# Kernel tuning notes

Hardware: AMD Instinct MI355X
Metric: run time of the kernel (lower is better)

The kernel has to match this reference:

```python
import jax, jax.numpy as jnp
import numpy as np

B, DIM, EMBDIM = 32, 512, 512
MEMSIZE, MEMSEQ = 32, 64
VOCAB = 50257


def setup_inputs() -> dict:
    key = jax.random.key(0)
    ks = jax.random.split(key, 10)
    inp = {
        'enc': jax.random.normal(ks[0], (B, DIM), jnp.float32),
        'encsumm': jax.random.normal(ks[1], (B, DIM), jnp.float32),
        'embsumm': jax.random.normal(ks[2], (B, EMBDIM), jnp.float32),
        'memencs': jax.random.normal(ks[3], (B, MEMSIZE, MEMSEQ, DIM), jnp.float32),
        'memencsumm': jax.random.normal(ks[4], (B, MEMSIZE, MEMSEQ, DIM), jnp.float32),
        'memembsumm': jax.random.normal(ks[5], (B, MEMSIZE, MEMSEQ, EMBDIM), jnp.float32),
        'memmask': jnp.ones((B, MEMSIZE, MEMSEQ), jnp.float32),
        'memids': jax.random.randint(ks[6], (B, MEMSIZE, MEMSEQ), 0, VOCAB, jnp.int64 if jax.config.jax_enable_x64 else jnp.int32),
        'W_out': jax.random.normal(ks[7], (VOCAB, 2 * DIM), jnp.float32) * 0.02,
        'b_out': jnp.zeros((VOCAB,), jnp.float32),
        'W_mix': jax.random.normal(ks[8], (2, 2 * DIM), jnp.float32) * 0.02,
        'b_mix': jnp.zeros((2,), jnp.float32),
        'unktok_mask': jnp.ones((VOCAB,), jnp.float32),  # no unktoks
    }
    return inp


def reference(enc, encsumm, embsumm, memencs, memencsumm, memembsumm, memmask,
              memids, W_out, b_out, W_mix, b_mix, unktok_mask):
    # copy branch: attention over flattened memory, scatter-add into vocab
    query = jnp.concatenate([embsumm, jnp.zeros_like(encsumm), enc], axis=-1)        # (B, 2*dim+embdim)
    keys = jnp.concatenate([memembsumm, jnp.zeros_like(memencsumm), memencs], axis=-1)  # (B, M, Z, 2*dim+embdim)
    w = jnp.einsum('bd,bmzd->bmz', query, keys) + jnp.log(memmask)
    b = w.shape[0]
    w = w.reshape(b, -1)                                    # (B, M*Z)
    alphas = jax.nn.softmax(w, axis=-1)
    mem_flat = memencs.reshape(b, -1, memencs.shape[-1])    # (B, M*Z, dim)
    mem_enc_summ = jnp.einsum('bm,bmd->bd', alphas, mem_flat)
    toks = memids.reshape(b, -1)                            # (B, M*Z)
    rows = jnp.arange(b)[:, None]
    vocsize = W_out.shape[0]
    probs_mem = jnp.zeros((b, vocsize), alphas.dtype).at[rows, toks].add(alphas)
    # generation branch
    h = jnp.concatenate([encsumm, enc], axis=-1)            # (B, 2*dim)
    logits_gen = h @ W_out.T + b_out + jnp.log(unktok_mask)[None, :]
    probs_gen = jax.nn.softmax(logits_gen, axis=-1)
    # mixer combine
    mix = jax.nn.softmax(h @ W_mix.T + b_mix, axis=-1)      # (B, 2)
    probs = mix[:, 0:1] * probs_gen + mix[:, 1:2] * probs_mem
    # original stack/gather trick: selects probs where nonzero, zeros where zero -> identity
    probs = jnp.where(probs != 0, probs, jnp.zeros_like(probs))
    return probs, mem_enc_summ
```

## Files before the change

### kernel.cpp

```cpp
#include <hip/hip_runtime.h>
#include <hip/hip_bf16.h>

#define NB   32
#define DIMK 512
#define MM   32
#define ZZ   64
#define MZV  2048
#define VOC  50257

typedef __attribute__((ext_vector_type(8))) short  short8;
typedef __attribute__((ext_vector_type(4))) float  f32x4;
typedef __attribute__((ext_vector_type(8))) unsigned short ushort8;

#define WS_W      0
#define WS_PVEC   (WS_W + NB*MZV)
#define WS_LSTAT  (WS_PVEC + NB*MM*DIMK)
#define WS_GSTATW (WS_LSTAT + NB*MM*2)
#define WS_MIX    (WS_GSTATW + NB*2)
#define WS_GPART  (WS_MIX + NB*2)
#define WS_H      (WS_GPART + NB*32*2)

__device__ __forceinline__ ushort8 cvt8(float4 a, float4 b) {
    union { ushort8 u; __hip_bfloat162 h[4]; } r;
    r.h[0] = __float22bfloat162_rn(make_float2(a.x, a.y));
    r.h[1] = __float22bfloat162_rn(make_float2(a.z, a.w));
    r.h[2] = __float22bfloat162_rn(make_float2(b.x, b.y));
    r.h[3] = __float22bfloat162_rn(make_float2(b.z, b.w));
    return r.u;
}

typedef const __attribute__((address_space(1))) void* gas_t;
typedef __attribute__((address_space(3))) void*       las_t;
__device__ __forceinline__ void gload16(const void* g, void* l) {
    __builtin_amdgcn_global_load_lds((gas_t)g, (las_t)l, 16, 0, 0);
}

__global__ void k0_stageh(const float* __restrict__ encsumm, const float* __restrict__ enc,
                          float* __restrict__ ws)
{
    int b = blockIdx.x;
    int c = threadIdx.x * 4;
    const float* src = (c < DIMK) ? (encsumm + b*DIMK + c) : (enc + b*DIMK + (c - DIMK));
    float4 v = *(const float4*)src;
    union { ushort4 u; __hip_bfloat162 h[2]; } o;
    o.h[0] = __float22bfloat162_rn(make_float2(v.x, v.y));
    o.h[1] = __float22bfloat162_rn(make_float2(v.z, v.w));
    *(ushort4*)((unsigned short*)(ws + WS_H) + b*1024 + c) = o.u;
}

__global__ __launch_bounds__(256) void k1_mem(
    const float* __restrict__ enc, const float* __restrict__ embsumm,
    const float* __restrict__ memencs, const float* __restrict__ memembsumm,
    const float* __restrict__ memmask, float* __restrict__ ws)
{
    int blk = blockIdx.x;
    int b = blk >> 5, m = blk & 31;
    int tid = threadIdx.x, wid = tid >> 6, lane = tid & 63;
    int c0 = lane * 4, c1 = c0 + 256;
    const float* encb = enc + b * DIMK;
    const float* embb = embsumm + b * DIMK;
    float4 qe0 = *(const float4*)(encb + c0);
    float4 qe1 = *(const float4*)(encb + c1);
    float4 qm0 = *(const float4*)(embb + c0);
    float4 qm1 = *(const float4*)(embb + c1);
    const float* meb = memencs    + (long)(b*MM + m) * ZZ * DIMK;
    const float* mmb = memembsumm + (long)(b*MM + m) * ZZ * DIMK;
    const float* mkb = memmask    + (long)(b*MM + m) * ZZ;
    float* w_ws = ws + WS_W + b*MZV + m*ZZ;

    float lmax = -3.0e38f, lsum = 0.f;
    float4 a0 = make_float4(0.f,0.f,0.f,0.f), a1 = make_float4(0.f,0.f,0.f,0.f);

    for (int z = wid; z < ZZ; z += 4) {
        const float* mer = meb + z*DIMK;
        const float* mmr = mmb + z*DIMK;
        float4 e0 = *(const float4*)(mer + c0);
        float4 e1 = *(const float4*)(mer + c1);
        float4 s0 = *(const float4*)(mmr + c0);
        float4 s1 = *(const float4*)(mmr + c1);
        float d = e0.x*qe0.x + e0.y*qe0.y + e0.z*qe0.z + e0.w*qe0.w
                + e1.x*qe1.x + e1.y*qe1.y + e1.z*qe1.z + e1.w*qe1.w
                + s0.x*qm0.x + s0.y*qm0.y + s0.z*qm0.z + s0.w*qm0.w
                + s1.x*qm1.x + s1.y*qm1.y + s1.z*qm1.z + s1.w*qm1.w;
        #pragma unroll
        for (int off = 32; off; off >>= 1) d += __shfl_xor(d, off);
        d += logf(mkb[z]);
        if (lane == 0) w_ws[z] = d;
        float nm = fmaxf(lmax, d);
        float sc = __expf(lmax - nm);
        float e  = __expf(d - nm);
        lsum = lsum * sc + e;
        a0.x = a0.x*sc + e*e0.x; a0.y = a0.y*sc + e*e0.y;
        a0.z = a0.z*sc + e*e0.z; a0.w = a0.w*sc + e*e0.w;
        a1.x = a1.x*sc + e*e1.x; a1.y = a1.y*sc + e*e1.y;
        a1.z = a1.z*sc + e*e1.z; a1.w = a1.w*sc + e*e1.w;
        lmax = nm;
    }

    __shared__ float sacc[4][DIMK];
    __shared__ float sst[4][2];
    *(float4*)&sacc[wid][c0] = a0;
    *(float4*)&sacc[wid][c1] = a1;
    if (lane == 0) { sst[wid][0] = lmax; sst[wid][1] = lsum; }
    __syncthreads();
    float bm = fmaxf(fmaxf(sst[0][0], sst[1][0]), fmaxf(sst[2][0], sst[3][0]));
    float sc0 = __expf(sst[0][0]-bm), sc1 = __expf(sst[1][0]-bm);
    float sc2 = __expf(sst[2][0]-bm), sc3 = __expf(sst[3][0]-bm);
    float bs = sst[0][1]*sc0 + sst[1][1]*sc1 + sst[2][1]*sc2 + sst[3][1]*sc3;
    int d0 = tid * 2;
    float2 v0 = *(float2*)&sacc[0][d0];
    float2 v1 = *(float2*)&sacc[1][d0];
    float2 v2 = *(float2*)&sacc[2][d0];
    float2 v3 = *(float2*)&sacc[3][d0];
    float p0 = v0.x*sc0 + v1.x*sc1 + v2.x*sc2 + v3.x*sc3;
    float p1 = v0.y*sc0 + v1.y*sc1 + v2.y*sc2 + v3.y*sc3;
    float* pv = ws + WS_PVEC + (long)(b*MM+m)*DIMK + d0;
    pv[0] = p0; pv[1] = p1;
    if (tid == 0) { float* ls = ws + WS_LSTAT + (b*MM+m)*2; ls[0] = bm; ls[1] = bs; }
}

__global__ __launch_bounds__(256) void k2_comb(
    const float* __restrict__ encsumm, const float* __restrict__ enc,
    const float* __restrict__ W_mix, const float* __restrict__ b_mix,
    float* __restrict__ out, float* __restrict__ ws)
{
    int b = blockIdx.x, tid = threadIdx.x;
    const float* ls = ws + WS_LSTAT + b*MM*2;
    float gm = -3.0e38f;
    #pragma unroll
    for (int m = 0; m < MM; m++) gm = fmaxf(gm, ls[m*2]);
    float gs = 0.f;
    #pragma unroll
    for (int m = 0; m < MM; m++) gs += ls[m*2+1] * __expf(ls[m*2] - gm);
    if (tid == 0) { ws[WS_GSTATW + b*2] = gm; ws[WS_GSTATW + b*2 + 1] = gs; }
    float inv = 1.0f / gs;
    int d0 = tid * 2;
    float p0 = 0.f, p1 = 0.f;
    for (int m = 0; m < MM; m++) {
        float sc = __expf(ls[m*2] - gm);
        const float* pv = ws + WS_PVEC + (long)(b*MM+m)*DIMK + d0;
        p0 += pv[0]*sc; p1 += pv[1]*sc;
    }
    out[(long)NB*VOC + b*DIMK + d0]     = p0 * inv;
    out[(long)NB*VOC + b*DIMK + d0 + 1] = p1 * inv;

    if (tid < 64) {
        int l = tid;
        float m0 = 0.f, m1 = 0.f;
        #pragma unroll
        for (int p = 0; p < 4; p++) {
            int cc = l*4 + p*256;
            float4 h4 = (cc < 512) ? *(const float4*)(encsumm + b*DIMK + cc)
                                   : *(const float4*)(enc + b*DIMK + cc - 512);
            float4 w0 = *(const float4*)(W_mix + cc);
            float4 w1 = *(const float4*)(W_mix + 1024 + cc);
            m0 += h4.x*w0.x + h4.y*w0.y + h4.z*w0.z + h4.w*w0.w;
            m1 += h4.x*w1.x + h4.y*w1.y + h4.z*w1.z + h4.w*w1.w;
        }
        #pragma unroll
        for (int off = 32; off; off >>= 1) { m0 += __shfl_xor(m0, off); m1 += __shfl_xor(m1, off); }
        if (l == 0) {
            m0 += b_mix[0]; m1 += b_mix[1];
            float mx = fmaxf(m0, m1);
            float e0 = __expf(m0-mx), e1 = __expf(m1-mx);
            float s = e0 + e1;
            ws[WS_MIX + b*2] = e0/s; ws[WS_MIX + b*2 + 1] = e1/s;
        }
    }
}

__global__ __launch_bounds__(256, 6) void k4_gemm(
    const unsigned short* __restrict__ hbf,
    const float* __restrict__ W_out, const float* __restrict__ b_out,
    const float* __restrict__ unk, float* __restrict__ logits)
{
    __shared__ __align__(16) float          w_lds[2][32*64];
    __shared__ __align__(16) unsigned short a_lds[2][32*64];
    int tid = threadIdx.x, wid = tid >> 6, lane = tid & 63;
    int wv = wid >> 1, wb = wid & 1;
    int vt = blockIdx.x * 32;

    int idx0 = (wid*2 + 0)*64 + lane;
    int idx1 = (wid*2 + 1)*64 + lane;
    int wr0 = idx0 >> 4, wq0 = idx0 & 15;
    int wr1 = idx1 >> 4, wq1 = idx1 & 15;
    const float* wsrc0 = W_out + (long)min(vt + wr0, VOC-1)*1024 + ((wq0 ^ (wr0 & 7))*4);
    const float* wsrc1 = W_out + (long)min(vt + wr1, VOC-1)*1024 + ((wq1 ^ (wr1 & 7))*4);
    int aidx = wid*64 + lane;
    int ar = aidx >> 3, ag = aidx & 7;
    const unsigned short* asrc = hbf + ar*1024 + ((ag ^ (ar & 7))*8);

#define ISSUE(c, buf) do {                                        \
        gload16(wsrc0 + (c)*64, &w_lds[buf][idx0*4]);             \
        gload16(wsrc1 + (c)*64, &w_lds[buf][idx1*4]);             \
        gload16(asrc  + (c)*64, &a_lds[buf][aidx*8]); } while (0)

    int lg = lane >> 4, ln = lane & 15;
    int vrow = wv*16 + ln;
    int ab   = wb*16 + ln;
    f32x4 acc = {0.f, 0.f, 0.f, 0.f};

    ISSUE(0, 0);
    ISSUE(1, 1);
    __syncthreads();

    for (int c = 0; c < 16; ++c) {
        int buf = c & 1;
        #pragma unroll
        for (int s = 0; s < 2; ++s) {
            int q = s*8 + lg*2;
            float4 b0 = *(const float4*)&w_lds[buf][vrow*64 + ((q    ) ^ (vrow & 7))*4];
            float4 b1 = *(const float4*)&w_lds[buf][vrow*64 + ((q + 1) ^ (vrow & 7))*4];
            int g = s*4 + lg;
            short8 afrag = *(const short8*)&a_lds[buf][ab*64 + ((g ^ (ab & 7)))*8];
            ushort8 bu = cvt8(b0, b1);
            short8 bfrag = *(short8*)&bu;
            acc = __builtin_amdgcn_mfma_f32_16x16x32_bf16(afrag, bfrag, acc, 0, 0, 0);
        }
        __syncthreads();
        if (c + 2 < 16) ISSUE(c + 2, buf);
    }
#undef ISSUE

    int v = vt + vrow;
    if (v < VOC) {
        float bias = b_out[v] + logf(unk[v]);
        #pragma unroll
        for (int rr = 0; rr < 4; ++rr) {
            int m = wb*16 + lg*4 + rr;
            logits[(long)m*VOC + v] = acc[rr] + bias;
        }
    }
}

__global__ __launch_bounds__(256) void k5_gstat(const float* __restrict__ logits, float* __restrict__ ws)
{
    int chunk = blockIdx.x, b = blockIdx.y, tid = threadIdx.x;
    const int CH = (VOC + 31) / 32;
    int v0 = chunk * CH;
    int v1 = min(VOC, v0 + CH);
    float m = -3.0e38f, s = 0.f;
    for (int v = v0 + tid; v < v1; v += 256) {
        float x = logits[(long)b*VOC + v];
        float nm = fmaxf(m, x);
        s = s*__expf(m - nm) + __expf(x - nm);
        m = nm;
    }
    #pragma unroll
    for (int off = 32; off; off >>= 1) {
        float om = __shfl_xor(m, off), os = __shfl_xor(s, off);
        float nm = fmaxf(m, om);
        s = s*__expf(m - nm) + os*__expf(om - nm);
        m = nm;
    }
    __shared__ float sm[4], ssum[4];
    int wid = tid >> 6, lane = tid & 63;
    if (lane == 0) { sm[wid] = m; ssum[wid] = s; }
    __syncthreads();
    if (tid == 0) {
        float gm = fmaxf(fmaxf(sm[0], sm[1]), fmaxf(sm[2], sm[3]));
        float gs = ssum[0]*__expf(sm[0]-gm) + ssum[1]*__expf(sm[1]-gm)
                 + ssum[2]*__expf(sm[2]-gm) + ssum[3]*__expf(sm[3]-gm);
        ws[WS_GPART + (b*32 + chunk)*2]     = gm;
        ws[WS_GPART + (b*32 + chunk)*2 + 1] = gs;
    }
}

__global__ __launch_bounds__(256) void k6_final(float* __restrict__ probs, const float* __restrict__ ws)
{
    int v = blockIdx.x*256 + threadIdx.x;
    int b = blockIdx.y;
    float gm = -3.0e38f;
    #pragma unroll
    for (int i = 0; i < 32; ++i) gm = fmaxf(gm, ws[WS_GPART + (b*32+i)*2]);
    float gs = 0.f;
    #pragma unroll
    for (int i = 0; i < 32; ++i)
        gs += ws[WS_GPART + (b*32+i)*2 + 1] * __expf(ws[WS_GPART + (b*32+i)*2] - gm);
    if (v >= VOC) return;
    float mix0 = ws[WS_MIX + b*2];
    long idx = (long)b*VOC + v;
    probs[idx] = mix0 * __expf(probs[idx] - gm) / gs;
}

__global__ __launch_bounds__(256) void k7_scatter(const int* __restrict__ memids,
                                                  const float* __restrict__ ws,
                                                  float* __restrict__ probs)
{
    int idx = blockIdx.x*256 + threadIdx.x;
    int b = idx >> 11, mz = idx & 2047;
    float gm = ws[WS_GSTATW + b*2], gs = ws[WS_GSTATW + b*2 + 1];
    float mix1 = ws[WS_MIX + b*2 + 1];
    float alpha = __expf(ws[WS_W + b*MZV + mz] - gm) / gs;
    int tok = memids[b*MZV + mz];
    atomicAdd(&probs[(long)b*VOC + tok], mix1 * alpha);
}

extern "C" void kernel_launch(void* const* d_in, const int* in_sizes, int n_in,
                              void* d_out, int out_size, void* d_ws, size_t ws_size,
                              hipStream_t stream)
{
    const float* enc        = (const float*)d_in[0];
    const float* encsumm    = (const float*)d_in[1];
    const float* embsumm    = (const float*)d_in[2];
    const float* memencs    = (const float*)d_in[3];
    const float* memembsumm = (const float*)d_in[5];
    const float* memmask    = (const float*)d_in[6];
    const int*   memids     = (const int*)d_in[7];
    const float* W_out      = (const float*)d_in[8];
    const float* b_out      = (const float*)d_in[9];
    const float* W_mix      = (const float*)d_in[10];
    const float* b_mix      = (const float*)d_in[11];
    const float* unk        = (const float*)d_in[12];
    float* out = (float*)d_out;
    float* ws  = (float*)d_ws;

    hipLaunchKernelGGL(k0_stageh, dim3(NB), dim3(256), 0, stream, encsumm, enc, ws);
    hipLaunchKernelGGL(k1_mem, dim3(NB*MM), dim3(256), 0, stream,
                       enc, embsumm, memencs, memembsumm, memmask, ws);
    hipLaunchKernelGGL(k2_comb, dim3(NB), dim3(256), 0, stream,
                       encsumm, enc, W_mix, b_mix, out, ws);
    hipLaunchKernelGGL(k4_gemm, dim3((VOC + 31)/32), dim3(256), 0, stream,
                       (const unsigned short*)(ws + WS_H), W_out, b_out, unk, out);
    hipLaunchKernelGGL(k5_gstat, dim3(32, NB), dim3(256), 0, stream, out, ws);
    hipLaunchKernelGGL(k6_final, dim3((VOC + 255)/256, NB), dim3(256), 0, stream, out, ws);
    hipLaunchKernelGGL(k7_scatter, dim3(NB*MZV/256), dim3(256), 0, stream, memids, ws, out);
}
```

Baseline: 141.5 us.

## Fuse memory-attention and vocab GEMM kernels into one interleaved launch

Merges the memory attention kernel and the output-projection GEMM into a single kernel whose blocks are interleaved: even block ids in the first 2048 do attention work, odd ones and the rest do GEMM tiles, with a shared-memory union. The aim is to run the two independent memory-bound phases concurrently so both streams of HBM traffic overlap and one launch gap disappears. The launch bound hint drops from 6 to 4 blocks per CU for the GEMM path, which may reduce its occupancy, and the k2_comb ordering now follows the fused kernel. Correctness relies on k2_comb not reading the GEMM output, which it does not, since the GEMM writes only logits.

```diff
diff --git a/kernel.cpp b/kernel.cpp
--- a/kernel.cpp
+++ b/kernel.cpp
@@ -7,6 +7,7 @@
 #define ZZ   64
 #define MZV  2048
 #define VOC  50257
+#define NK4  1571
 
 typedef __attribute__((ext_vector_type(8))) short  short8;
 typedef __attribute__((ext_vector_type(4))) float  f32x4;
@@ -48,75 +49,145 @@
     *(ushort4*)((unsigned short*)(ws + WS_H) + b*1024 + c) = o.u;
 }
 
-__global__ __launch_bounds__(256) void k1_mem(
+__global__ __launch_bounds__(256, 4) void k14_fused(
     const float* __restrict__ enc, const float* __restrict__ embsumm,
     const float* __restrict__ memencs, const float* __restrict__ memembsumm,
-    const float* __restrict__ memmask, float* __restrict__ ws)
-{
-    int blk = blockIdx.x;
-    int b = blk >> 5, m = blk & 31;
+    const float* __restrict__ memmask,
+    const unsigned short* __restrict__ hbf,
+    const float* __restrict__ W_out, const float* __restrict__ b_out,
+    const float* __restrict__ unk, float* __restrict__ out,
+    float* __restrict__ ws)
+{
+    __shared__ __align__(16) union {
+        struct { float sacc[4][DIMK]; float sst[4][2]; } s1;
+        struct { float w[2][2048]; unsigned short a[2][2048]; } s4;
+    } smem;
+
+    int bid = blockIdx.x;
     int tid = threadIdx.x, wid = tid >> 6, lane = tid & 63;
-    int c0 = lane * 4, c1 = c0 + 256;
-    const float* encb = enc + b * DIMK;
-    const float* embb = embsumm + b * DIMK;
-    float4 qe0 = *(const float4*)(encb + c0);
-    float4 qe1 = *(const float4*)(encb + c1);
-    float4 qm0 = *(const float4*)(embb + c0);
-    float4 qm1 = *(const float4*)(embb + c1);
-    const float* meb = memencs    + (long)(b*MM + m) * ZZ * DIMK;
-    const float* mmb = memembsumm + (long)(b*MM + m) * ZZ * DIMK;
-    const float* mkb = memmask    + (long)(b*MM + m) * ZZ;
-    float* w_ws = ws + WS_W + b*MZV + m*ZZ;
-
-    float lmax = -3.0e38f, lsum = 0.f;
-    float4 a0 = make_float4(0.f,0.f,0.f,0.f), a1 = make_float4(0.f,0.f,0.f,0.f);
-
-    for (int z = wid; z < ZZ; z += 4) {
-        const float* mer = meb + z*DIMK;
-        const float* mmr = mmb + z*DIMK;
-        float4 e0 = *(const float4*)(mer + c0);
-        float4 e1 = *(const float4*)(mer + c1);
-        float4 s0 = *(const float4*)(mmr + c0);
-        float4 s1 = *(const float4*)(mmr + c1);
-        float d = e0.x*qe0.x + e0.y*qe0.y + e0.z*qe0.z + e0.w*qe0.w
-                + e1.x*qe1.x + e1.y*qe1.y + e1.z*qe1.z + e1.w*qe1.w
-                + s0.x*qm0.x + s0.y*qm0.y + s0.z*qm0.z + s0.w*qm0.w
-                + s1.x*qm1.x + s1.y*qm1.y + s1.z*qm1.z + s1.w*qm1.w;
-        #pragma unroll
-        for (int off = 32; off; off >>= 1) d += __shfl_xor(d, off);
-        d += logf(mkb[z]);
-        if (lane == 0) w_ws[z] = d;
-        float nm = fmaxf(lmax, d);
-        float sc = __expf(lmax - nm);
-        float e  = __expf(d - nm);
-        lsum = lsum * sc + e;
-        a0.x = a0.x*sc + e*e0.x; a0.y = a0.y*sc + e*e0.y;
-        a0.z = a0.z*sc + e*e0.z; a0.w = a0.w*sc + e*e0.w;
-        a1.x = a1.x*sc + e*e1.x; a1.y = a1.y*sc + e*e1.y;
-        a1.z = a1.z*sc + e*e1.z; a1.w = a1.w*sc + e*e1.w;
-        lmax = nm;
-    }
-
-    __shared__ float sacc[4][DIMK];
-    __shared__ float sst[4][2];
-    *(float4*)&sacc[wid][c0] = a0;
-    *(float4*)&sacc[wid][c1] = a1;
-    if (lane == 0) { sst[wid][0] = lmax; sst[wid][1] = lsum; }
-    __syncthreads();
-    float bm = fmaxf(fmaxf(sst[0][0], sst[1][0]), fmaxf(sst[2][0], sst[3][0]));
-    float sc0 = __expf(sst[0][0]-bm), sc1 = __expf(sst[1][0]-bm);
-    float sc2 = __expf(sst[2][0]-bm), sc3 = __expf(sst[3][0]-bm);
-    float bs = sst[0][1]*sc0 + sst[1][1]*sc1 + sst[2][1]*sc2 + sst[3][1]*sc3;
-    int d0 = tid * 2;
-    float2 v0 = *(float2*)&sacc[0][d0];
-    float2 v1 = *(float2*)&sacc[1][d0];
-    float2 v2 = *(float2*)&sacc[2][d0];
-    float2 v3 = *(float2*)&sacc[3][d0];
-    float p0 = v0.x*sc0 + v1.x*sc1 + v2.x*sc2 + v3.x*sc3;
-    float p1 = v0.y*sc0 + v1.y*sc1 + v2.y*sc2 + v3.y*sc3;
-    float* pv = ws + WS_PVEC + (long)(b*MM+m)*DIMK + d0;
-    pv[0] = p0; pv[1] = p1;
-    if (tid == 0) { float* ls = ws + WS_LSTAT + (b*MM+m)*2; ls[0] = bm; ls[1] = bs; }
+    bool isK1; int sub;
+    if (bid < 2048) { isK1 = ((bid & 1) == 0); sub = bid >> 1; }
+    else            { isK1 = false;            sub = bid - 1024; }
+
+    if (isK1) {
+        int b = sub >> 5, m = sub & 31;
+        int c0 = lane * 4, c1 = c0 + 256;
+        const float* encb = enc + b * DIMK;
+        const float* embb = embsumm + b * DIMK;
+        float4 qe0 = *(const float4*)(encb + c0);
+        float4 qe1 = *(const float4*)(encb + c1);
+        float4 qm0 = *(const float4*)(embb + c0);
+        float4 qm1 = *(const float4*)(embb + c1);
+        const float* meb = memencs    + (long)(b*MM + m) * ZZ * DIMK;
+        const float* mmb = memembsumm + (long)(b*MM + m) * ZZ * DIMK;
+        const float* mkb = memmask    + (long)(b*MM + m) * ZZ;
+        float* w_ws = ws + WS_W + b*MZV + m*ZZ;
+
+        float lmax = -3.0e38f, lsum = 0.f;
+        float4 a0 = make_float4(0.f,0.f,0.f,0.f), a1 = make_float4(0.f,0.f,0.f,0.f);
+
+        for (int z = wid; z < ZZ; z += 4) {
+            const float* mer = meb + z*DIMK;
+            const float* mmr = mmb + z*DIMK;
+            float4 e0 = *(const float4*)(mer + c0);
+            float4 e1 = *(const float4*)(mer + c1);
+            float4 s0 = *(const float4*)(mmr + c0);
+            float4 s1 = *(const float4*)(mmr + c1);
+            float d = e0.x*qe0.x + e0.y*qe0.y + e0.z*qe0.z + e0.w*qe0.w
+                    + e1.x*qe1.x + e1.y*qe1.y + e1.z*qe1.z + e1.w*qe1.w
+                    + s0.x*qm0.x + s0.y*qm0.y + s0.z*qm0.z + s0.w*qm0.w
+                    + s1.x*qm1.x + s1.y*qm1.y + s1.z*qm1.z + s1.w*qm1.w;
+            #pragma unroll
+            for (int off = 32; off; off >>= 1) d += __shfl_xor(d, off);
+            d += logf(mkb[z]);
+            if (lane == 0) w_ws[z] = d;
+            float nm = fmaxf(lmax, d);
+            float sc = __expf(lmax - nm);
+            float e  = __expf(d - nm);
+            lsum = lsum * sc + e;
+            a0.x = a0.x*sc + e*e0.x; a0.y = a0.y*sc + e*e0.y;
+            a0.z = a0.z*sc + e*e0.z; a0.w = a0.w*sc + e*e0.w;
+            a1.x = a1.x*sc + e*e1.x; a1.y = a1.y*sc + e*e1.y;
+            a1.z = a1.z*sc + e*e1.z; a1.w = a1.w*sc + e*e1.w;
+            lmax = nm;
+        }
+
+        *(float4*)&smem.s1.sacc[wid][c0] = a0;
+        *(float4*)&smem.s1.sacc[wid][c1] = a1;
+        if (lane == 0) { smem.s1.sst[wid][0] = lmax; smem.s1.sst[wid][1] = lsum; }
+        __syncthreads();
+        float bm = fmaxf(fmaxf(smem.s1.sst[0][0], smem.s1.sst[1][0]),
+                         fmaxf(smem.s1.sst[2][0], smem.s1.sst[3][0]));
+        float sc0 = __expf(smem.s1.sst[0][0]-bm), sc1 = __expf(smem.s1.sst[1][0]-bm);
+        float sc2 = __expf(smem.s1.sst[2][0]-bm), sc3 = __expf(smem.s1.sst[3][0]-bm);
+        float bs = smem.s1.sst[0][1]*sc0 + smem.s1.sst[1][1]*sc1
+                 + smem.s1.sst[2][1]*sc2 + smem.s1.sst[3][1]*sc3;
+        int d0 = tid * 2;
+        float2 v0 = *(float2*)&smem.s1.sacc[0][d0];
+        float2 v1 = *(float2*)&smem.s1.sacc[1][d0];
+        float2 v2 = *(float2*)&smem.s1.sacc[2][d0];
+        float2 v3 = *(float2*)&smem.s1.sacc[3][d0];
+        float p0 = v0.x*sc0 + v1.x*sc1 + v2.x*sc2 + v3.x*sc3;
+        float p1 = v0.y*sc0 + v1.y*sc1 + v2.y*sc2 + v3.y*sc3;
+        float* pv = ws + WS_PVEC + (long)(b*MM+m)*DIMK + d0;
+        pv[0] = p0; pv[1] = p1;
+        if (tid == 0) { float* ls = ws + WS_LSTAT + (b*MM+m)*2; ls[0] = bm; ls[1] = bs; }
+    } else {
+        int wv = wid >> 1, wb = wid & 1;
+        int vt = sub * 32;
+
+        int idx0 = (wid*2 + 0)*64 + lane;
+        int idx1 = (wid*2 + 1)*64 + lane;
+        int wr0 = idx0 >> 4, wq0 = idx0 & 15;
+        int wr1 = idx1 >> 4, wq1 = idx1 & 15;
+        const float* wsrc0 = W_out + (long)min(vt + wr0, VOC-1)*1024 + ((wq0 ^ (wr0 & 7))*4);
+        const float* wsrc1 = W_out + (long)min(vt + wr1, VOC-1)*1024 + ((wq1 ^ (wr1 & 7))*4);
+        int aidx = wid*64 + lane;
+        int ar = aidx >> 3, ag = aidx & 7;
+        const unsigned short* asrc = hbf + ar*1024 + ((ag ^ (ar & 7))*8);
+
+#define ISSUE(c, buf) do {                                            \
+            gload16(wsrc0 + (c)*64, &smem.s4.w[buf][idx0*4]);         \
+            gload16(wsrc1 + (c)*64, &smem.s4.w[buf][idx1*4]);         \
+            gload16(asrc  + (c)*64, &smem.s4.a[buf][aidx*8]); } while (0)
+
+        int lg = lane >> 4, ln = lane & 15;
+        int vrow = wv*16 + ln;
+        int ab   = wb*16 + ln;
+        f32x4 acc = {0.f, 0.f, 0.f, 0.f};
+
+        ISSUE(0, 0);
+        ISSUE(1, 1);
+        __syncthreads();
+
+        for (int c = 0; c < 16; ++c) {
+            int buf = c & 1;
+            #pragma unroll
+            for (int s = 0; s < 2; ++s) {
+                int q = s*8 + lg*2;
+                float4 b0 = *(const float4*)&smem.s4.w[buf][vrow*64 + ((q    ) ^ (vrow & 7))*4];
+                float4 b1 = *(const float4*)&smem.s4.w[buf][vrow*64 + ((q + 1) ^ (vrow & 7))*4];
+                int g = s*4 + lg;
+                short8 afrag = *(const short8*)&smem.s4.a[buf][ab*64 + ((g ^ (ab & 7)))*8];
+                ushort8 bu = cvt8(b0, b1);
+                short8 bfrag = *(short8*)&bu;
+                acc = __builtin_amdgcn_mfma_f32_16x16x32_bf16(afrag, bfrag, acc, 0, 0, 0);
+            }
+            __syncthreads();
+            if (c + 2 < 16) ISSUE(c + 2, buf);
+        }
+#undef ISSUE
+
+        int v = vt + vrow;
+        if (v < VOC) {
+            float bias = b_out[v] + logf(unk[v]);
+            #pragma unroll
+            for (int rr = 0; rr < 4; ++rr) {
+                int m = wb*16 + lg*4 + rr;
+                out[(long)m*VOC + v] = acc[rr] + bias;
+            }
+        }
+    }
 }
 
 __global__ __launch_bounds__(256) void k2_comb(
@@ -165,70 +236,6 @@
             float e0 = __expf(m0-mx), e1 = __expf(m1-mx);
             float s = e0 + e1;
             ws[WS_MIX + b*2] = e0/s; ws[WS_MIX + b*2 + 1] = e1/s;
-        }
-    }
-}
-
-__global__ __launch_bounds__(256, 6) void k4_gemm(
-    const unsigned short* __restrict__ hbf,
-    const float* __restrict__ W_out, const float* __restrict__ b_out,
-    const float* __restrict__ unk, float* __restrict__ logits)
-{
-    __shared__ __align__(16) float          w_lds[2][32*64];
-    __shared__ __align__(16) unsigned short a_lds[2][32*64];
-    int tid = threadIdx.x, wid = tid >> 6, lane = tid & 63;
-    int wv = wid >> 1, wb = wid & 1;
-    int vt = blockIdx.x * 32;
-
-    int idx0 = (wid*2 + 0)*64 + lane;
-    int idx1 = (wid*2 + 1)*64 + lane;
-    int wr0 = idx0 >> 4, wq0 = idx0 & 15;
-    int wr1 = idx1 >> 4, wq1 = idx1 & 15;
-    const float* wsrc0 = W_out + (long)min(vt + wr0, VOC-1)*1024 + ((wq0 ^ (wr0 & 7))*4);
-    const float* wsrc1 = W_out + (long)min(vt + wr1, VOC-1)*1024 + ((wq1 ^ (wr1 & 7))*4);
-    int aidx = wid*64 + lane;
-    int ar = aidx >> 3, ag = aidx & 7;
-    const unsigned short* asrc = hbf + ar*1024 + ((ag ^ (ar & 7))*8);
-
-#define ISSUE(c, buf) do {                                        \
-        gload16(wsrc0 + (c)*64, &w_lds[buf][idx0*4]);             \
-        gload16(wsrc1 + (c)*64, &w_lds[buf][idx1*4]);             \
-        gload16(asrc  + (c)*64, &a_lds[buf][aidx*8]); } while (0)
-
-    int lg = lane >> 4, ln = lane & 15;
-    int vrow = wv*16 + ln;
-    int ab   = wb*16 + ln;
-    f32x4 acc = {0.f, 0.f, 0.f, 0.f};
-
-    ISSUE(0, 0);
-    ISSUE(1, 1);
-    __syncthreads();
-
-    for (int c = 0; c < 16; ++c) {
-        int buf = c & 1;
-        #pragma unroll
-        for (int s = 0; s < 2; ++s) {
-            int q = s*8 + lg*2;
-            float4 b0 = *(const float4*)&w_lds[buf][vrow*64 + ((q    ) ^ (vrow & 7))*4];
-            float4 b1 = *(const float4*)&w_lds[buf][vrow*64 + ((q + 1) ^ (vrow & 7))*4];
-            int g = s*4 + lg;
-            short8 afrag = *(const short8*)&a_lds[buf][ab*64 + ((g ^ (ab & 7)))*8];
-            ushort8 bu = cvt8(b0, b1);
-            short8 bfrag = *(short8*)&bu;
-            acc = __builtin_amdgcn_mfma_f32_16x16x32_bf16(afrag, bfrag, acc, 0, 0, 0);
-        }
-        __syncthreads();
-        if (c + 2 < 16) ISSUE(c + 2, buf);
-    }
-#undef ISSUE
-
-    int v = vt + vrow;
-    if (v < VOC) {
-        float bias = b_out[v] + logf(unk[v]);
-        #pragma unroll
-        for (int rr = 0; rr < 4; ++rr) {
-            int m = wb*16 + lg*4 + rr;
-            logits[(long)m*VOC + v] = acc[rr] + bias;
         }
     }
 }
@@ -316,12 +323,11 @@
     float* ws  = (float*)d_ws;
 
     hipLaunchKernelGGL(k0_stageh, dim3(NB), dim3(256), 0, stream, encsumm, enc, ws);
-    hipLaunchKernelGGL(k1_mem, dim3(NB*MM), dim3(256), 0, stream,
-                       enc, embsumm, memencs, memembsumm, memmask, ws);
+    hipLaunchKernelGGL(k14_fused, dim3(1024 + NK4), dim3(256), 0, stream,
+                       enc, embsumm, memencs, memembsumm, memmask,
+                       (const unsigned short*)(ws + WS_H), W_out, b_out, unk, out, ws);
     hipLaunchKernelGGL(k2_comb, dim3(NB), dim3(256), 0, stream,
                        encsumm, enc, W_mix, b_mix, out, ws);
-    hipLaunchKernelGGL(k4_gemm, dim3((VOC + 31)/32), dim3(256), 0, stream,
-                       (const unsigned short*)(ws + WS_H), W_out, b_out, unk, out);
     hipLaunchKernelGGL(k5_gstat, dim3(32, NB), dim3(256), 0, stream, out, ws);
     hipLaunchKernelGGL(k6_final, dim3((VOC + 255)/256, NB), dim3(256), 0, stream, out, ws);
     hipLaunchKernelGGL(k7_scatter, dim3(NB*MZV/256), dim3(256), 0, stream, memids, ws, out);
```

New measurement: 137.1 us. 3.1% less time.
